# Kernel tuning notes

Measured on AMD Instinct MI355X. Metric: run time of the kernel, lower is better.

The kernel has to match this reference:

```python
import jax, jax.numpy as jnp
import numpy as np

INDIM, OUTDIM, GRID_SIZE, K, BATCH = 128, 128, 5, 3, 1024


def setup_inputs() -> dict:
    key = jax.random.key(0)
    k1, k2 = jax.random.split(key)
    size = INDIM * OUTDIM
    x = jax.random.normal(k1, (BATCH, INDIM), dtype=jnp.float32)
    # grid = ones(size) outer linspace(grid_range, grid_size+1): (size, G+1)
    grid = jnp.broadcast_to(
        jnp.linspace(-1.0, 1.0, GRID_SIZE + 1, dtype=jnp.float32), (size, GRID_SIZE + 1)
    )
    # spline coefficients: (size, grid_size + spline_order)
    spline_weights = jax.random.normal(k2, (size, GRID_SIZE + K), dtype=jnp.float32) * 0.1
    c_spl = jnp.ones((size,), dtype=jnp.float32)
    c_res = jnp.ones((size,), dtype=jnp.float32)
    return {"x": x, "grid": grid, "spline_weights": spline_weights,
            "c_spl": c_spl, "c_res": c_res}


def b_spline_basis(x, grid, k):
    """Cox-de Boor B-spline basis (pykan B_batch).
    x: (size, batch), grid: (size, G+1) -> bases: (size, G+k, batch)."""
    h = (grid[:, -1:] - grid[:, :1]) / (grid.shape[1] - 1)
    # extend grid by k knots on each side
    for _ in range(k):
        grid = jnp.concatenate([grid[:, :1] - h, grid, grid[:, -1:] + h], axis=1)
    g = grid[:, :, None]          # (size, G_ext, 1)
    xe = x[:, None, :]            # (size, 1, batch)
    B = ((xe >= g[:, :-1]) & (xe < g[:, 1:])).astype(x.dtype)  # order-0 indicators
    for p in range(1, k + 1):
        B = (xe - g[:, :-(p + 1)]) / (g[:, p:-1] - g[:, :-(p + 1)]) * B[:, :-1] \
            + (g[:, p + 1:] - xe) / (g[:, p + 1:] - g[:, 1:-p]) * B[:, 1:]
    return B


def reference(x, grid, spline_weights, c_spl, c_res):
    batch = x.shape[0]
    size = grid.shape[0]
    # einsum('ij,k->ikj') + reshape + permute -> (size, batch), outdim-major
    x_e = jnp.broadcast_to(x[:, None, :], (batch, OUTDIM, INDIM)).reshape(batch, size).T
    res = jax.nn.silu(x_e).T                              # (batch, size)
    bi = b_spline_basis(x_e, grid, K)                     # (size, G+K, batch)
    spl = jnp.einsum('ij,ijk->ik', spline_weights, bi).T  # (batch, size)
    y = c_spl[None, :] * spl + c_res[None, :] * res       # (batch, size)
    y = y.reshape(batch, OUTDIM, INDIM).sum(axis=2) / INDIM  # (batch, outdim)
    grid_r = grid.reshape(OUTDIM, INDIM, -1)
    inp_norm = grid_r[:, :, -1] - grid_r[:, :, 0] + 1e-5
    spl_reg = jnp.mean(jnp.abs(spl.reshape(batch, OUTDIM, INDIM)), axis=0) / inp_norm
    return y, spl_reg
```

## Files before the change

kernel.cpp:

```cpp
#include <hip/hip_runtime.h>

#define INDIM  128
#define OUTDIM 128
#define GSZ    5
#define BATCH  1024
#define KTOT   1152
#define APAD   1160

typedef _Float16 half_t;
typedef _Float16 half8 __attribute__((ext_vector_type(8)));
typedef float    f32x4 __attribute__((ext_vector_type(4)));

#define BH2_OFF  (BATCH * KTOT)
#define WC_OFF   (BH2_OFF + INDIM * BATCH * 8)

__device__ __forceinline__ half8 basis8(float x, float g0, float g5) {
    const float h  = (g5 - g0) * (1.0f / GSZ);
    const float e0 = ((g0 - h) - h) - h;
    const float xb = (x - e0) * (1.0f / h);
    const float jf = floorf(xb);
    const int   j0 = (int)jf;
    const float u  = xb - jf;
    const float t1 = 1.0f - u;
    const float u2 = u * u, u3 = u2 * u;
    const float c0 = t1 * t1 * t1 * (1.0f / 6.0f);
    const float c1 = fmaf(0.5f, u3, fmaf(-1.0f, u2, 2.0f / 3.0f));
    const float c2 = fmaf(-0.5f, u3, fmaf(0.5f, u2, fmaf(0.5f, u, 1.0f / 6.0f)));
    const float c3 = u3 * (1.0f / 6.0f);
    half8 bs = {0, 0, 0, 0, 0, 0, 0, 0};
#pragma unroll
    for (int k = 0; k < 8; ++k) {
        const int d = k - j0 + 3;
        const float v = (d == 0) ? c0 : (d == 1) ? c1 : (d == 2) ? c2 : (d == 3) ? c3 : 0.0f;
        bs[k] = (half_t)v;
    }
    return bs;
}

__device__ __forceinline__ half8 cvt8(float4 a, float4 b, float s) {
    half8 r;
    r[0] = (half_t)(s * a.x); r[1] = (half_t)(s * a.y);
    r[2] = (half_t)(s * a.z); r[3] = (half_t)(s * a.w);
    r[4] = (half_t)(s * b.x); r[5] = (half_t)(s * b.y);
    r[6] = (half_t)(s * b.z); r[7] = (half_t)(s * b.w);
    return r;
}

__global__ __launch_bounds__(256) void k_prep(
    const float* __restrict__ X, const float* __restrict__ G,
    const float* __restrict__ W, const float* __restrict__ Csp,
    const float* __restrict__ Cre, half_t* __restrict__ ws)
{
    const int bid = blockIdx.x, t = threadIdx.x;
    if (bid < 512) {
        const int in = bid >> 2;
        const int b  = ((bid & 3) << 8) + t;
        const float g0 = G[in * 6 + 0], g5 = G[in * 6 + 5];
        const half8 bs = basis8(X[b * INDIM + in], g0, g5);
        *(half8*)&ws[BH2_OFF + in * (BATCH * 8) + b * 8] = bs;
    } else if (bid < 1024) {
        const int gid = (bid - 512) * 256 + t;
        const int b = gid >> 7, in = gid & 127;
        const float x  = X[gid];
        const float g0 = G[in * 6 + 0], g5 = G[in * 6 + 5];
        *(half8*)&ws[b * KTOT + in * 8] = basis8(x, g0, g5);
        ws[b * KTOT + 1024 + in] = (half_t)(x / (1.0f + __expf(-x)));
    } else {
        const int sp = (bid - 1024) * 256 + t;
        const int in = sp >> 7, o = sp & 127;
        const int s  = o * INDIM + in;
        const float4 w0 = *(const float4*)&W[s * 8];
        const float4 w1 = *(const float4*)&W[s * 8 + 4];
        *(half8*)&ws[WC_OFF + (in * 128 + o) * 8] = cvt8(w0, w1, Csp[s]);
        ws[WC_OFF + ((128 + (in >> 3)) * 128 + o) * 8 + (in & 7)] = (half_t)Cre[s];
    }
}

__global__ __launch_bounds__(256) void k_main(
    const float* __restrict__ G, const float* __restrict__ W,
    const half_t* __restrict__ ws,
    float* __restrict__ Y, float* __restrict__ REG)
{
    __shared__ __align__(16) unsigned char smem[16 * APAD * 2];
    const int bid = blockIdx.x, t = threadIdx.x;
    const int w = t >> 6, lane = t & 63;
    const int col = lane & 15, quad = lane >> 4;
    const f32x4 zero4 = {0.f, 0.f, 0.f, 0.f};

    if (bid < 128) {
        half_t (*A)[APAD] = (half_t (*)[APAD])smem;
        const int m0 = (bid >> 1) * 16;
        const int nh = bid & 1;
#pragma unroll
        for (int idx = t; idx < 16 * 144; idx += 256) {
            const int r = idx / 144, c = idx % 144;
            *(half8*)&A[r][c * 8] = *(const half8*)&ws[(m0 + r) * KTOT + c * 8];
        }
        __syncthreads();

        const int o = nh * 64 + w * 16 + col;
        f32x4 acc = zero4;
#pragma unroll 6
        for (int kt = 0; kt < 36; ++kt) {
            const half8 a = *(const half8*)&A[col][kt * 32 + quad * 8];
            const half8 b = *(const half8*)&ws[WC_OFF + ((kt * 4 + quad) * 128 + o) * 8];
            acc = __builtin_amdgcn_mfma_f32_16x16x32_f16(a, b, acc, 0, 0, 0);
        }
#pragma unroll
        for (int r = 0; r < 4; ++r)
            Y[(m0 + quad * 4 + r) * OUTDIM + o] = acc[r] * (1.0f / INDIM);
    } else {
        float* SH = (float*)smem;
        const int rb = bid - 128;
        const int in = rb & 127;
        const int o0 = (rb >> 7) * 16;

        half8 bfrag = {0, 0, 0, 0, 0, 0, 0, 0};
        if (quad == 0) {
            const int s = (o0 + col) * INDIM + in;
            const float4 w0 = *(const float4*)&W[s * 8];
            const float4 w1 = *(const float4*)&W[s * 8 + 4];
            bfrag = cvt8(w0, w1, 1.0f);
        }
        float r0 = 0.f, r1 = 0.f, r2 = 0.f, r3 = 0.f;
#pragma unroll 4
        for (int bt = w; bt < 64; bt += 4) {
            half8 a = {0, 0, 0, 0, 0, 0, 0, 0};
            if (quad == 0)
                a = *(const half8*)&ws[BH2_OFF + in * (BATCH * 8) + (bt * 16 + col) * 8];
            const f32x4 c = __builtin_amdgcn_mfma_f32_16x16x32_f16(a, bfrag, zero4, 0, 0, 0);
            r0 += fabsf(c[0]); r1 += fabsf(c[1]); r2 += fabsf(c[2]); r3 += fabsf(c[3]);
        }
        float sum = (r0 + r1) + (r2 + r3);
        sum += __shfl_xor(sum, 16);
        sum += __shfl_xor(sum, 32);
        if (lane < 16) SH[w * 16 + lane] = sum;
        __syncthreads();
        if (t < 16) {
            const int s = (o0 + t) * INDIM + in;
            const float gg0 = G[s * 6], gg5 = G[s * 6 + 5];
            REG[s] = (SH[t] + SH[16 + t] + SH[32 + t] + SH[48 + t])
                     * (1.0f / BATCH) / (gg5 - gg0 + 1e-5f);
        }
    }
}

extern "C" void kernel_launch(void* const* d_in, const int* in_sizes, int n_in,
                              void* d_out, int out_size, void* d_ws, size_t ws_size,
                              hipStream_t stream) {
    const float* X   = (const float*)d_in[0];
    const float* G   = (const float*)d_in[1];
    const float* W   = (const float*)d_in[2];
    const float* Csp = (const float*)d_in[3];
    const float* Cre = (const float*)d_in[4];
    float* Y   = (float*)d_out;
    float* REG = (float*)d_out + BATCH * OUTDIM;
    half_t* ws = (half_t*)d_ws;

    k_prep<<<1088, 256, 0, stream>>>(X, G, W, Csp, Cre, ws);
    k_main<<<1152, 256, 0, stream>>>(G, W, ws, Y, REG);
}
```

Measured before the change: 20.89 us.

## Unify basis workspace into K-chunk-major layout and drop LDS staging

```diff
diff --git a/kernel.cpp b/kernel.cpp
--- a/kernel.cpp
+++ b/kernel.cpp
@@ -4,15 +4,13 @@
 #define OUTDIM 128
 #define GSZ    5
 #define BATCH  1024
-#define KTOT   1152
-#define APAD   1160
+#define KC     144
 
 typedef _Float16 half_t;
 typedef _Float16 half8 __attribute__((ext_vector_type(8)));
 typedef float    f32x4 __attribute__((ext_vector_type(4)));
 
-#define BH2_OFF  (BATCH * KTOT)
-#define WC_OFF   (BH2_OFF + INDIM * BATCH * 8)
+#define WC2_OFF  (KC * BATCH * 8)
 
 __device__ __forceinline__ half8 basis8(float x, float g0, float g5) {
     const float h  = (g5 - g0) * (1.0f / GSZ);
@@ -55,24 +53,19 @@
     if (bid < 512) {
         const int in = bid >> 2;
         const int b  = ((bid & 3) << 8) + t;
+        const float x  = X[b * INDIM + in];
         const float g0 = G[in * 6 + 0], g5 = G[in * 6 + 5];
-        const half8 bs = basis8(X[b * INDIM + in], g0, g5);
-        *(half8*)&ws[BH2_OFF + in * (BATCH * 8) + b * 8] = bs;
-    } else if (bid < 1024) {
-        const int gid = (bid - 512) * 256 + t;
-        const int b = gid >> 7, in = gid & 127;
-        const float x  = X[gid];
-        const float g0 = G[in * 6 + 0], g5 = G[in * 6 + 5];
-        *(half8*)&ws[b * KTOT + in * 8] = basis8(x, g0, g5);
-        ws[b * KTOT + 1024 + in] = (half_t)(x / (1.0f + __expf(-x)));
+        *(half8*)&ws[(in * BATCH + b) * 8] = basis8(x, g0, g5);
+        ws[((128 + (in >> 3)) * BATCH + b) * 8 + (in & 7)] =
+            (half_t)(x / (1.0f + __expf(-x)));
     } else {
-        const int sp = (bid - 1024) * 256 + t;
+        const int sp = (bid - 512) * 256 + t;
         const int in = sp >> 7, o = sp & 127;
         const int s  = o * INDIM + in;
         const float4 w0 = *(const float4*)&W[s * 8];
         const float4 w1 = *(const float4*)&W[s * 8 + 4];
-        *(half8*)&ws[WC_OFF + (in * 128 + o) * 8] = cvt8(w0, w1, Csp[s]);
-        ws[WC_OFF + ((128 + (in >> 3)) * 128 + o) * 8 + (in & 7)] = (half_t)Cre[s];
+        *(half8*)&ws[WC2_OFF + (in * 128 + o) * 8] = cvt8(w0, w1, Csp[s]);
+        ws[WC2_OFF + ((128 + (in >> 3)) * 128 + o) * 8 + (in & 7)] = (half_t)Cre[s];
     }
 }
 
@@ -81,36 +74,28 @@
     const half_t* __restrict__ ws,
     float* __restrict__ Y, float* __restrict__ REG)
 {
-    __shared__ __align__(16) unsigned char smem[16 * APAD * 2];
+    __shared__ float SH[64];
     const int bid = blockIdx.x, t = threadIdx.x;
     const int w = t >> 6, lane = t & 63;
     const int col = lane & 15, quad = lane >> 4;
     const f32x4 zero4 = {0.f, 0.f, 0.f, 0.f};
 
     if (bid < 128) {
-        half_t (*A)[APAD] = (half_t (*)[APAD])smem;
         const int m0 = (bid >> 1) * 16;
         const int nh = bid & 1;
-#pragma unroll
-        for (int idx = t; idx < 16 * 144; idx += 256) {
-            const int r = idx / 144, c = idx % 144;
-            *(half8*)&A[r][c * 8] = *(const half8*)&ws[(m0 + r) * KTOT + c * 8];
-        }
-        __syncthreads();
-
-        const int o = nh * 64 + w * 16 + col;
+        const int o  = nh * 64 + w * 16 + col;
         f32x4 acc = zero4;
 #pragma unroll 6
         for (int kt = 0; kt < 36; ++kt) {
-            const half8 a = *(const half8*)&A[col][kt * 32 + quad * 8];
-            const half8 b = *(const half8*)&ws[WC_OFF + ((kt * 4 + quad) * 128 + o) * 8];
+            const int kc = kt * 4 + quad;
+            const half8 a = *(const half8*)&ws[(kc * BATCH + m0 + col) * 8];
+            const half8 b = *(const half8*)&ws[WC2_OFF + (kc * 128 + o) * 8];
             acc = __builtin_amdgcn_mfma_f32_16x16x32_f16(a, b, acc, 0, 0, 0);
         }
 #pragma unroll
         for (int r = 0; r < 4; ++r)
             Y[(m0 + quad * 4 + r) * OUTDIM + o] = acc[r] * (1.0f / INDIM);
     } else {
-        float* SH = (float*)smem;
         const int rb = bid - 128;
         const int in = rb & 127;
         const int o0 = (rb >> 7) * 16;
@@ -127,7 +112,7 @@
         for (int bt = w; bt < 64; bt += 4) {
             half8 a = {0, 0, 0, 0, 0, 0, 0, 0};
             if (quad == 0)
-                a = *(const half8*)&ws[BH2_OFF + in * (BATCH * 8) + (bt * 16 + col) * 8];
+                a = *(const half8*)&ws[(in * BATCH + bt * 16 + col) * 8];
             const f32x4 c = __builtin_amdgcn_mfma_f32_16x16x32_f16(a, bfrag, zero4, 0, 0, 0);
             r0 += fabsf(c[0]); r1 += fabsf(c[1]); r2 += fabsf(c[2]); r3 += fabsf(c[3]);
         }
@@ -157,6 +142,6 @@
     float* REG = (float*)d_out + BATCH * OUTDIM;
     half_t* ws = (half_t*)d_ws;
 
-    k_prep<<<1088, 256, 0, stream>>>(X, G, W, Csp, Cre, ws);
+    k_prep<<<576, 256, 0, stream>>>(X, G, W, Csp, Cre, ws);
     k_main<<<1152, 256, 0, stream>>>(G, W, ws, Y, REG);
 }
```

Result: faster. 18.16 us, median of 2 (-13.1%).
